# Kernel optimization log

Hardware: AMD Instinct MI355X
Metric: run time of the kernel (lower is better)

The kernel has to match this reference:

```python
import jax, jax.numpy as jnp
import numpy as np

MAX_NUM_LEVELS = 3.5
NUM_LEVELS = 4  # mip levels 0..3 (levels clamped to [0, 2.5])


def affine_grid(matrix, N, H, W):
    # F.affine_grid, align_corners=False. matrix: (N,2,3) -> grid (N,H,W,2) in xy order.
    xs = (jnp.arange(W, dtype=jnp.float32) + 0.5) * (2.0 / W) - 1.0
    ys = (jnp.arange(H, dtype=jnp.float32) + 0.5) * (2.0 / H) - 1.0
    gy, gx = jnp.meshgrid(ys, xs, indexing='ij')
    base = jnp.stack([gx, gy, jnp.ones_like(gx)], axis=-1)  # (H,W,3)
    return jnp.einsum('hwk,nik->nhwi', base, matrix)  # (N,H,W,2)


def grid_sample_border(img, grid):
    # bilinear grid_sample, padding_mode='border', align_corners=False
    N, C, H, W = img.shape
    x = (grid[..., 0] + 1.0) * (W / 2.0) - 0.5
    y = (grid[..., 1] + 1.0) * (H / 2.0) - 0.5
    x0 = jnp.floor(x); y0 = jnp.floor(y)
    tx = x - x0; ty = y - y0
    x0i = jnp.clip(x0.astype(jnp.int32), 0, W - 1)
    x1i = jnp.clip(x0.astype(jnp.int32) + 1, 0, W - 1)
    y0i = jnp.clip(y0.astype(jnp.int32), 0, H - 1)
    y1i = jnp.clip(y0.astype(jnp.int32) + 1, 0, H - 1)
    b = jnp.arange(N)[:, None, None]
    g = lambda yi, xi: img[b, :, yi, xi]  # (N,Ho,Wo,C) gather
    out = (g(y0i, x0i) * ((1 - tx) * (1 - ty))[..., None]
           + g(y0i, x1i) * (tx * (1 - ty))[..., None]
           + g(y1i, x0i) * ((1 - tx) * ty)[..., None]
           + g(y1i, x1i) * (tx * ty)[..., None])
    return jnp.transpose(out, (0, 3, 1, 2))  # (N,C,Ho,Wo)


def blur_downsample(x):
    N, C, H, W = x.shape
    k1 = jnp.array([1., 3., 3., 1.], dtype=x.dtype) / 8.0
    k = k1[:, None] * k1[None, :]
    xp = jnp.pad(x, ((0, 0), (0, 0), (1, 2), (1, 2)), mode='reflect')
    kernel = jnp.broadcast_to(k[None, None], (C, 1, 4, 4))
    return jax.lax.conv_general_dilated(xp, kernel, window_strides=(2, 2), padding='VALID',
                                        feature_group_count=C,
                                        dimension_numbers=('NCHW', 'OIHW', 'NCHW'))


def compute_levels(grid, H, W):
    # per-pixel mip LOD from local stretch of the sampling grid (in source pixel units)
    coords = (grid + 1.0) * 0.5 * jnp.array([W, H], dtype=grid.dtype)  # (N,Ho,Wo,2)
    dx = coords[:, :-1, 1:] - coords[:, :-1, :-1]
    dy = coords[:, 1:, :-1] - coords[:, :-1, :-1]
    scale = jnp.maximum(jnp.linalg.norm(dx, axis=-1), jnp.linalg.norm(dy, axis=-1))
    scale = jnp.pad(scale, ((0, 0), (0, 1), (0, 1)), mode='edge')  # (N,Ho,Wo)
    levels = jnp.log2(jnp.maximum(scale, 1.0))
    return jnp.clip(levels, 0.0, MAX_NUM_LEVELS - 1.0)


def mipmap_warp(img, grid):
    N, C, H, W = img.shape
    levels = compute_levels(grid, H, W)  # (N,Ho,Wo)
    pyr = [img]
    for _ in range(NUM_LEVELS - 1):
        pyr.append(blur_downsample(pyr[-1]))
    samples = jnp.stack([grid_sample_border(p, grid) for p in pyr], axis=0)  # (L,N,C,Ho,Wo)
    ls = jnp.arange(NUM_LEVELS, dtype=levels.dtype)[:, None, None, None]
    w = jnp.clip(1.0 - jnp.abs(levels[None] - ls), 0.0, 1.0)  # trilinear blend weights (L,N,Ho,Wo)
    return jnp.einsum('lnhw,lnchw->nchw', w, samples)


def setup_inputs() -> dict:
    key = jax.random.key(0)
    k1, k2, k3 = jax.random.split(key, 3)
    N, C, H, W, D = 64, 3, 256, 256, 512
    img = jax.random.normal(k1, (N, C, H, W), dtype=jnp.float32)
    features = jax.random.normal(k2, (N, D), dtype=jnp.float32)
    # learned head params (zero-init in torch; small random here so the warp is nontrivial)
    lin_w = jax.random.normal(k3, (4, D), dtype=jnp.float32) * 0.02
    lin_b = jnp.zeros((4,), dtype=jnp.float32)
    return {'img': img, 'features': features, 'lin_w': lin_w, 'lin_b': lin_b}


def reference(img, features, lin_w, lin_b):
    params = features @ lin_w.T + lin_b  # (N,4)
    rot = jnp.tanh(params[:, 0:1]) * jnp.pi
    scale = jnp.exp(params[:, 1:2])
    sx, sy = params[:, 2:3], params[:, 3:4]
    c, s = jnp.cos(rot), jnp.sin(rot)
    matrix = jnp.concatenate([scale * c, -scale * s, sx, scale * s, scale * c, sy], axis=1).reshape(-1, 2, 3)
    affine_params = jnp.concatenate([rot, scale, sx, sy], axis=1)
    N, C, H, W = img.shape
    grid = affine_grid(matrix, N, H, W)
    out = mipmap_warp(img, grid)
    return out, grid, matrix, affine_params
```

## Files before the change

### kernel.cpp

```cpp
#include <hip/hip_runtime.h>
#include <math.h>

#define N_B 64
#define C_CH 3
#define H_IMG 256
#define W_IMG 256
#define D_FEAT 512

#define OUT_OFF_GRID   12582912
#define OUT_OFF_MATRIX 20971520
#define OUT_OFF_AFFINE 20971904

#define PYR1_SZ (N_B * 128 * 128 * 3)
#define PYR2_SZ (N_B * 64 * 64 * 3)
#define PYR3_SZ (N_B * 32 * 32 * 3)

typedef float v2f __attribute__((ext_vector_type(2)));
typedef float v4f __attribute__((ext_vector_type(4)));
typedef float f4u __attribute__((ext_vector_type(4), aligned(4)));
typedef float f2u __attribute__((ext_vector_type(2), aligned(4)));

__global__ void params_kernel(const float* __restrict__ features,
                              const float* __restrict__ lin_w,
                              const float* __restrict__ lin_b,
                              float* __restrict__ out_matrix,
                              float* __restrict__ out_affine,
                              float* __restrict__ ws_params)
{
    const int n = blockIdx.x;
    const int t = threadIdx.x;
    const float* f = features + n * D_FEAT;
    float f0 = f[t];
    float f1 = f[t + 256];
    float a0 = f0 * lin_w[0 * D_FEAT + t] + f1 * lin_w[0 * D_FEAT + t + 256];
    float a1 = f0 * lin_w[1 * D_FEAT + t] + f1 * lin_w[1 * D_FEAT + t + 256];
    float a2 = f0 * lin_w[2 * D_FEAT + t] + f1 * lin_w[2 * D_FEAT + t + 256];
    float a3 = f0 * lin_w[3 * D_FEAT + t] + f1 * lin_w[3 * D_FEAT + t + 256];

    __shared__ float red[4][256];
    red[0][t] = a0; red[1][t] = a1; red[2][t] = a2; red[3][t] = a3;
    __syncthreads();
    for (int s = 128; s > 0; s >>= 1) {
        if (t < s) {
            red[0][t] += red[0][t + s];
            red[1][t] += red[1][t + s];
            red[2][t] += red[2][t + s];
            red[3][t] += red[3][t + s];
        }
        __syncthreads();
    }
    if (t == 0) {
        float p0 = red[0][0] + lin_b[0];
        float p1 = red[1][0] + lin_b[1];
        float p2 = red[2][0] + lin_b[2];
        float p3 = red[3][0] + lin_b[3];
        float rot   = tanhf(p0) * 3.14159265358979323846f;
        float scale = expf(p1);
        float c = cosf(rot), s = sinf(rot);
        float m00 = scale * c, m01 = -scale * s, m02 = p2;
        float m10 = scale * s, m11 =  scale * c, m12 = p3;
        out_matrix[n * 6 + 0] = m00;
        out_matrix[n * 6 + 1] = m01;
        out_matrix[n * 6 + 2] = m02;
        out_matrix[n * 6 + 3] = m10;
        out_matrix[n * 6 + 4] = m11;
        out_matrix[n * 6 + 5] = m12;
        out_affine[n * 4 + 0] = rot;
        out_affine[n * 4 + 1] = scale;
        out_affine[n * 4 + 2] = p2;
        out_affine[n * 4 + 3] = p3;
        float lv = log2f(fmaxf(scale, 1.0f));
        lv = fminf(fmaxf(lv, 0.0f), 2.5f);
        ws_params[n * 8 + 0] = m00;
        ws_params[n * 8 + 1] = m01;
        ws_params[n * 8 + 2] = m02;
        ws_params[n * 8 + 3] = m10;
        ws_params[n * 8 + 4] = m11;
        ws_params[n * 8 + 5] = m12;
        ws_params[n * 8 + 6] = lv;
        ws_params[n * 8 + 7] = 0.0f;
    }
}

__global__ void down1_kernel(const float* __restrict__ img,
                             float* __restrict__ pyr1,
                             const float* __restrict__ ws_params)
{
    const int n = blockIdx.y;
    if (ws_params[n * 8 + 6] <= 0.0f) return;
    const int p = blockIdx.x * 256 + threadIdx.x;
    const int i = p >> 7;
    const int j = p & 127;

    int r[4];
#pragma unroll
    for (int a = 0; a < 4; a++) {
        int q = 2 * i + a - 1;
        if (q < 0) q = -q;
        if (q >= 256) q = 510 - q;
        r[a] = q;
    }
    const int  cb  = min(max(2 * j - 1, 0), 252);
    const bool jlo = (j == 0);
    const bool jhi = (j == 127);
    const bool je  = jlo || jhi;

    const float* s = img + (size_t)n * 3 * 65536;

    f4u T[3][4];
#pragma unroll
    for (int c = 0; c < 3; c++)
#pragma unroll
        for (int a = 0; a < 4; a++)
            T[c][a] = *(const f4u*)(s + c * 65536 + r[a] * 256 + cb);

    const float k0 = 0.125f, k1 = 0.375f;
    const float kr[4] = {0.125f, 0.375f, 0.375f, 0.125f};
    float o[3];
#pragma unroll
    for (int c = 0; c < 3; c++) {
        float acc = 0.0f;
#pragma unroll
        for (int a = 0; a < 4; a++) {
            f4u A = T[c][a];
            float t0 = je  ? A.y : A.x;
            float t1 = jlo ? A.x : (jhi ? A.z : A.y);
            float t2 = jlo ? A.y : (jhi ? A.w : A.z);
            float t3 = je  ? A.z : A.w;
            float h = k0 * t0 + k1 * t1 + k1 * t2 + k0 * t3;
            acc += kr[a] * h;
        }
        o[c] = acc;
    }
    float* d = pyr1 + (size_t)n * (128 * 128 * 3) + (size_t)p * 3;
    d[0] = o[0]; d[1] = o[1]; d[2] = o[2];
}

template<int Hs, int Ws>
__global__ void downN_kernel(const float* __restrict__ src,
                             float* __restrict__ dst,
                             const float* __restrict__ ws_params,
                             float lvl_gate)
{
    const int n = blockIdx.y;
    if (ws_params[n * 8 + 6] <= lvl_gate) return;
    constexpr int Hd = Hs / 2, Wd = Ws / 2;
    const int p = blockIdx.x * 256 + threadIdx.x;
    const int i = p / Wd;
    const int j = p % Wd;

    int r[4], cc[4];
#pragma unroll
    for (int a = 0; a < 4; a++) {
        int q = 2 * i + a - 1;
        if (q < 0) q = -q;
        if (q >= Hs) q = 2 * Hs - 2 - q;
        r[a] = q;
        int u = 2 * j + a - 1;
        if (u < 0) u = -u;
        if (u >= Ws) u = 2 * Ws - 2 - u;
        cc[a] = u;
    }
    const float* s = src + (size_t)n * 3 * Hs * Ws;
    const int rs = 3 * Ws;

    f4u T[4][4];
#pragma unroll
    for (int a = 0; a < 4; a++)
#pragma unroll
        for (int b = 0; b < 4; b++)
            T[a][b] = *(const f4u*)(s + r[a] * rs + 3 * cc[b]);

    const float k0 = 0.125f, k1 = 0.375f;
    const float kr[4] = {0.125f, 0.375f, 0.375f, 0.125f};
    float o[3];
#pragma unroll
    for (int c = 0; c < 3; c++) {
        float acc = 0.0f;
#pragma unroll
        for (int a = 0; a < 4; a++) {
            float h = k0 * T[a][0][c] + k1 * T[a][1][c]
                    + k1 * T[a][2][c] + k0 * T[a][3][c];
            acc += kr[a] * h;
        }
        o[c] = acc;
    }
    float* d = dst + (size_t)n * 3 * Hd * Wd + (size_t)p * 3;
    d[0] = o[0]; d[1] = o[1]; d[2] = o[2];
}

struct TapSetup {
    const float* row0;
    const float* row1;
    float w00, w01, w10, w11;
    bool selHi0, selLo1;
    size_t planeStride;
};

__device__ __forceinline__ TapSetup make_taps(const float* __restrict__ base, int l,
                                              float X, float Y)
{
    const int Wl = W_IMG >> l;
    const int Hl = H_IMG >> l;
    float x = (X + 1.0f) * (0.5f * (float)Wl) - 0.5f;
    float y = (Y + 1.0f) * (0.5f * (float)Hl) - 0.5f;
    float x0f = floorf(x), y0f = floorf(y);
    float tx = x - x0f, ty = y - y0f;
    int x0 = (int)x0f, y0 = (int)y0f;
    int y0i = min(max(y0,     0), Hl - 1);
    int y1i = min(max(y0 + 1, 0), Hl - 1);
    int xp = min(max(x0, 0), Wl - 2);
    TapSetup ts;
    ts.row0 = base + (size_t)y0i * Wl + xp;
    ts.row1 = base + (size_t)y1i * Wl + xp;
    ts.selHi0 = (x0 >= Wl - 1);
    ts.selLo1 = (x0 < 0);
    ts.w00 = (1.0f - tx) * (1.0f - ty);
    ts.w01 = tx * (1.0f - ty);
    ts.w10 = (1.0f - tx) * ty;
    ts.w11 = tx * ty;
    ts.planeStride = (size_t)Hl * Wl;
    return ts;
}

__device__ __forceinline__ float tap_eval(const TapSetup& ts, float2 a, float2 b)
{
    float t00 = ts.selHi0 ? a.y : a.x;
    float t01 = ts.selLo1 ? a.x : a.y;
    float t10 = ts.selHi0 ? b.y : b.x;
    float t11 = ts.selLo1 ? b.x : b.y;
    return ts.w00 * t00 + ts.w01 * t01 + ts.w10 * t10 + ts.w11 * t11;
}

struct NTap {
    const float* r0;
    const float* r1;
    float w00, w01, w10, w11;
    bool hi, lo;
};

__device__ __forceinline__ NTap make_ntap(const float* __restrict__ base, int l,
                                          float X, float Y)
{
    const int Wl = W_IMG >> l;
    const int Hl = H_IMG >> l;
    float x = (X + 1.0f) * (0.5f * (float)Wl) - 0.5f;
    float y = (Y + 1.0f) * (0.5f * (float)Hl) - 0.5f;
    float x0f = floorf(x), y0f = floorf(y);
    float tx = x - x0f, ty = y - y0f;
    int x0 = (int)x0f, y0 = (int)y0f;
    int y0i = min(max(y0,     0), Hl - 1);
    int y1i = min(max(y0 + 1, 0), Hl - 1);
    int xp  = min(max(x0, 0), Wl - 2);
    const int rs = 3 * Wl;
    NTap t;
    t.r0 = base + (size_t)y0i * rs + 3 * xp;
    t.r1 = base + (size_t)y1i * rs + 3 * xp;
    t.hi = (x0 >= Wl - 1);
    t.lo = (x0 < 0);
    t.w00 = (1.0f - tx) * (1.0f - ty);
    t.w01 = tx * (1.0f - ty);
    t.w10 = (1.0f - tx) * ty;
    t.w11 = tx * ty;
    return t;
}

struct NPay { f4u a; f2u a2; f4u b; f2u b2; };

__device__ __forceinline__ NPay ntap_load(const NTap& t)
{
    NPay p;
    p.a  = *(const f4u*)t.r0;  p.a2 = *(const f2u*)(t.r0 + 4);
    p.b  = *(const f4u*)t.r1;  p.b2 = *(const f2u*)(t.r1 + 4);
    return p;
}

__device__ __forceinline__ void ntap_eval(const NTap& t, const NPay& p, float* v)
{
    float e0[6] = {p.a.x, p.a.y, p.a.z, p.a.w, p.a2.x, p.a2.y};
    float e1[6] = {p.b.x, p.b.y, p.b.z, p.b.w, p.b2.x, p.b2.y};
#pragma unroll
    for (int c = 0; c < 3; c++) {
        float p00 = t.hi ? e0[c + 3] : e0[c];
        float p01 = t.lo ? e0[c]     : e0[c + 3];
        float p10 = t.hi ? e1[c + 3] : e1[c];
        float p11 = t.lo ? e1[c]     : e1[c + 3];
        v[c] = t.w00 * p00 + t.w01 * p01 + t.w10 * p10 + t.w11 * p11;
    }
}

__device__ __forceinline__ const float* npyr(int l, const float* p1,
                                             const float* p2, const float* p3,
                                             int n)
{
    if (l == 1) return p1 + (size_t)n * (128 * 128 * 3);
    if (l == 2) return p2 + (size_t)n * (64 * 64 * 3);
    return p3 + (size_t)n * (32 * 32 * 3);
}

__global__ __launch_bounds__(256, 4)
void warp_kernel(const float* __restrict__ img,
                 const float* __restrict__ pyr1,
                 const float* __restrict__ pyr2,
                 const float* __restrict__ pyr3,
                 const float* __restrict__ ws_params,
                 float* __restrict__ out,
                 float* __restrict__ gridOut)
{
    const int n = blockIdx.y;
    const int tile = blockIdx.x;
    const int tid = threadIdx.x;
    const int w0 = (tile & 7) << 5;
    const int h0 = (tile >> 3) << 4;
    const int w  = w0 + ((tid & 15) << 1);
    const int h  = h0 + (tid >> 4);

    const float* P = ws_params + n * 8;
    float m00 = P[0], m01 = P[1], m02 = P[2];
    float m10 = P[3], m11 = P[4], m12 = P[5];
    float lv  = P[6];

    float gxa = ((float)w + 0.5f) * (2.0f / (float)W_IMG) - 1.0f;
    float gxb = ((float)(w + 1) + 0.5f) * (2.0f / (float)W_IMG) - 1.0f;
    float gy  = ((float)h + 0.5f) * (2.0f / (float)H_IMG) - 1.0f;
    float Xa = m00 * gxa + m01 * gy + m02;
    float Ya = m10 * gxa + m11 * gy + m12;
    float Xb = m00 * gxb + m01 * gy + m02;
    float Yb = m10 * gxb + m11 * gy + m12;

    v4f gp = {Xa, Ya, Xb, Yb};
    __builtin_nontemporal_store(gp,
        (v4f*)(gridOut + ((size_t)(n * H_IMG + h) * W_IMG + w) * 2));

    int   l0   = (int)lv;
    float frac = lv - (float)l0;
    const bool hasL1 = (frac > 0.0f);
    const float wA = 1.0f - frac;

    size_t obase = ((size_t)n * C_CH * H_IMG + h) * W_IMG + w;

    if (l0 == 0) {
        const float* base0 = img + (size_t)n * 3 * 65536;
        TapSetup ta = make_taps(base0, 0, Xa, Ya);
        TapSetup tb = make_taps(base0, 0, Xb, Yb);
        float2 Aa[3], Ba[3], Ab[3], Bb[3];
#pragma unroll
        for (int c = 0; c < 3; c++) {
            Aa[c] = *(const float2*)(ta.row0 + c * 65536);
            Ba[c] = *(const float2*)(ta.row1 + c * 65536);
            Ab[c] = *(const float2*)(tb.row0 + c * 65536);
            Bb[c] = *(const float2*)(tb.row1 + c * 65536);
        }
        if (hasL1) {
            const float* b1 = pyr1 + (size_t)n * (128 * 128 * 3);
            NTap ua = make_ntap(b1, 1, Xa, Ya);
            NTap ub = make_ntap(b1, 1, Xb, Yb);
            NPay pa = ntap_load(ua);
            NPay pb = ntap_load(ub);
            float v1a[3], v1b[3];
            ntap_eval(ua, pa, v1a);
            ntap_eval(ub, pb, v1b);
#pragma unroll
            for (int c = 0; c < 3; c++) {
                float v0a = tap_eval(ta, Aa[c], Ba[c]);
                float v0b = tap_eval(tb, Ab[c], Bb[c]);
                v2f o2 = {wA * v0a + frac * v1a[c], wA * v0b + frac * v1b[c]};
                __builtin_nontemporal_store(o2,
                    (v2f*)(out + obase + (size_t)c * 65536));
            }
        } else {
#pragma unroll
            for (int c = 0; c < 3; c++) {
                v2f o2 = {tap_eval(ta, Aa[c], Ba[c]), tap_eval(tb, Ab[c], Bb[c])};
                __builtin_nontemporal_store(o2,
                    (v2f*)(out + obase + (size_t)c * 65536));
            }
        }
    } else {
        const float* base0 = npyr(l0, pyr1, pyr2, pyr3, n);
        NTap ta = make_ntap(base0, l0, Xa, Ya);
        NTap tb = make_ntap(base0, l0, Xb, Yb);
        NPay pa = ntap_load(ta);
        NPay pb = ntap_load(tb);
        if (hasL1) {
            const float* base1 = npyr(l0 + 1, pyr1, pyr2, pyr3, n);
            NTap ua = make_ntap(base1, l0 + 1, Xa, Ya);
            NTap ub = make_ntap(base1, l0 + 1, Xb, Yb);
            NPay qa = ntap_load(ua);
            NPay qb = ntap_load(ub);
            float v0a[3], v0b[3], v1a[3], v1b[3];
            ntap_eval(ta, pa, v0a);
            ntap_eval(tb, pb, v0b);
            ntap_eval(ua, qa, v1a);
            ntap_eval(ub, qb, v1b);
#pragma unroll
            for (int c = 0; c < 3; c++) {
                v2f o2 = {wA * v0a[c] + frac * v1a[c], wA * v0b[c] + frac * v1b[c]};
                __builtin_nontemporal_store(o2,
                    (v2f*)(out + obase + (size_t)c * 65536));
            }
        } else {
            float v0a[3], v0b[3];
            ntap_eval(ta, pa, v0a);
            ntap_eval(tb, pb, v0b);
#pragma unroll
            for (int c = 0; c < 3; c++) {
                v2f o2 = {v0a[c], v0b[c]};
                __builtin_nontemporal_store(o2,
                    (v2f*)(out + obase + (size_t)c * 65536));
            }
        }
    }
}

extern "C" void kernel_launch(void* const* d_in, const int* in_sizes, int n_in,
                              void* d_out, int out_size, void* d_ws, size_t ws_size,
                              hipStream_t stream)
{
    const float* img      = (const float*)d_in[0];
    const float* features = (const float*)d_in[1];
    const float* lin_w    = (const float*)d_in[2];
    const float* lin_b    = (const float*)d_in[3];

    float* out        = (float*)d_out;
    float* gridOut    = out + OUT_OFF_GRID;
    float* out_matrix = out + OUT_OFF_MATRIX;
    float* out_affine = out + OUT_OFF_AFFINE;

    float* ws        = (float*)d_ws;
    float* ws_params = ws;
    float* pyr1 = ws + 1024;
    float* pyr2 = pyr1 + PYR1_SZ;
    float* pyr3 = pyr2 + PYR2_SZ;

    params_kernel<<<N_B, 256, 0, stream>>>(features, lin_w, lin_b,
                                           out_matrix, out_affine, ws_params);

    down1_kernel<<<dim3(64, N_B), 256, 0, stream>>>(img, pyr1, ws_params);
    downN_kernel<128, 128><<<dim3(16, N_B), 256, 0, stream>>>(pyr1, pyr2, ws_params, 1.0f);
    downN_kernel<64, 64><<<dim3(4, N_B), 256, 0, stream>>>(pyr2, pyr3, ws_params, 2.0f);

    warp_kernel<<<dim3(H_IMG * W_IMG / 512, N_B), 256, 0, stream>>>(
        img, pyr1, pyr2, pyr3, ws_params, out, gridOut);
}
```

Before: 164.5 us.

## Stage level-0 source footprint into LDS for warp tile bilinear sampling

For level-0 tiles, each block computes the bounding box of its 32x16 output tile's source footprint. If the box fits the 36 KB LDS buffer, the block cooperatively copies the three channel patches into LDS, synchronises, and does the bilinear taps from shared memory instead of scattered global float2 loads. The aim is to replace redundant, poorly coalesced gathers with coalesced row loads plus cheap LDS reads. In exchange it adds a __syncthreads, extra copy work when the footprint is large, and 36 KB of static LDS per block, which may cut occupancy below the launch_bounds target of 4 blocks.

```diff
diff --git a/kernel.cpp b/kernel.cpp
--- a/kernel.cpp
+++ b/kernel.cpp
@@ -14,6 +14,8 @@
 #define PYR1_SZ (N_B * 128 * 128 * 3)
 #define PYR2_SZ (N_B * 64 * 64 * 3)
 #define PYR3_SZ (N_B * 32 * 32 * 3)
+
+#define LDS_CAP 3072
 
 typedef float v2f __attribute__((ext_vector_type(2)));
 typedef float v4f __attribute__((ext_vector_type(4)));
@@ -232,6 +234,50 @@
     return ts.w00 * t00 + ts.w01 * t01 + ts.w10 * t10 + ts.w11 * t11;
 }
 
+struct STap {
+    int off0, off1;
+    float w00, w01, w10, w11;
+    bool hi, lo;
+};
+
+__device__ __forceinline__ STap make_stap(float X, float Y,
+                                          int bx0, int by0, int bwp)
+{
+    float x = (X + 1.0f) * 128.0f - 0.5f;
+    float y = (Y + 1.0f) * 128.0f - 0.5f;
+    float x0f = floorf(x), y0f = floorf(y);
+    float tx = x - x0f, ty = y - y0f;
+    int x0 = (int)x0f, y0 = (int)y0f;
+    int y0i = min(max(y0,     0), 255);
+    int y1i = min(max(y0 + 1, 0), 255);
+    int xp  = min(max(x0, 0), 254);
+    STap t;
+    t.off0 = (y0i - by0) * bwp + (xp - bx0);
+    t.off1 = (y1i - by0) * bwp + (xp - bx0);
+    t.hi = (x0 >= 255);
+    t.lo = (x0 < 0);
+    t.w00 = (1.0f - tx) * (1.0f - ty);
+    t.w01 = tx * (1.0f - ty);
+    t.w10 = (1.0f - tx) * ty;
+    t.w11 = tx * ty;
+    return t;
+}
+
+__device__ __forceinline__ void stap_eval(const float (*L)[LDS_CAP],
+                                          const STap& t, float* v)
+{
+#pragma unroll
+    for (int c = 0; c < 3; c++) {
+        f2u a = *(const f2u*)&L[c][t.off0];
+        f2u b = *(const f2u*)&L[c][t.off1];
+        float t00 = t.hi ? a.y : a.x;
+        float t01 = t.lo ? a.x : a.y;
+        float t10 = t.hi ? b.y : b.x;
+        float t11 = t.lo ? b.x : b.y;
+        v[c] = t.w00 * t00 + t.w01 * t01 + t.w10 * t10 + t.w11 * t11;
+    }
+}
+
 struct NTap {
     const float* r0;
     const float* r1;
@@ -307,6 +353,8 @@
                  float* __restrict__ out,
                  float* __restrict__ gridOut)
 {
+    __shared__ float lds[3][LDS_CAP];
+
     const int n = blockIdx.y;
     const int tile = blockIdx.x;
     const int tid = threadIdx.x;
@@ -340,38 +388,93 @@
     size_t obase = ((size_t)n * C_CH * H_IMG + h) * W_IMG + w;
 
     if (l0 == 0) {
-        const float* base0 = img + (size_t)n * 3 * 65536;
-        TapSetup ta = make_taps(base0, 0, Xa, Ya);
-        TapSetup tb = make_taps(base0, 0, Xb, Yb);
-        float2 Aa[3], Ba[3], Ab[3], Bb[3];
-#pragma unroll
-        for (int c = 0; c < 3; c++) {
-            Aa[c] = *(const float2*)(ta.row0 + c * 65536);
-            Ba[c] = *(const float2*)(ta.row1 + c * 65536);
-            Ab[c] = *(const float2*)(tb.row0 + c * 65536);
-            Bb[c] = *(const float2*)(tb.row1 + c * 65536);
-        }
+        float cgxl = ((float)w0 + 0.5f) * (2.0f / (float)W_IMG) - 1.0f;
+        float cgxr = ((float)(w0 + 31) + 0.5f) * (2.0f / (float)W_IMG) - 1.0f;
+        float cgyt = ((float)h0 + 0.5f) * (2.0f / (float)H_IMG) - 1.0f;
+        float cgyb = ((float)(h0 + 15) + 0.5f) * (2.0f / (float)H_IMG) - 1.0f;
+        float x00 = (m00 * cgxl + m01 * cgyt + m02 + 1.0f) * 128.0f - 0.5f;
+        float x01 = (m00 * cgxr + m01 * cgyt + m02 + 1.0f) * 128.0f - 0.5f;
+        float x10 = (m00 * cgxl + m01 * cgyb + m02 + 1.0f) * 128.0f - 0.5f;
+        float x11 = (m00 * cgxr + m01 * cgyb + m02 + 1.0f) * 128.0f - 0.5f;
+        float y00 = (m10 * cgxl + m11 * cgyt + m12 + 1.0f) * 128.0f - 0.5f;
+        float y01 = (m10 * cgxr + m11 * cgyt + m12 + 1.0f) * 128.0f - 0.5f;
+        float y10 = (m10 * cgxl + m11 * cgyb + m12 + 1.0f) * 128.0f - 0.5f;
+        float y11 = (m10 * cgxr + m11 * cgyb + m12 + 1.0f) * 128.0f - 0.5f;
+        float xmn = fminf(fminf(x00, x01), fminf(x10, x11));
+        float xmx = fmaxf(fmaxf(x00, x01), fmaxf(x10, x11));
+        float ymn = fminf(fminf(y00, y01), fminf(y10, y11));
+        float ymx = fmaxf(fmaxf(y00, y01), fmaxf(y10, y11));
+        int bx0 = min(max((int)floorf(xmn), 0), 255);
+        int bx1 = min(max((int)floorf(xmx) + 1, 0), 255);
+        int by0 = min(max((int)floorf(ymn), 0), 255);
+        int by1 = min(max((int)floorf(ymx) + 1, 0), 255);
+        int bw  = bx1 - bx0 + 1;
+        int bh  = by1 - by0 + 1;
+        int bwp = bw | 1;
+        const bool staged = (bh * bwp <= LDS_CAP);
+
+        NTap ua, ub; NPay pa, pb;
         if (hasL1) {
             const float* b1 = pyr1 + (size_t)n * (128 * 128 * 3);
-            NTap ua = make_ntap(b1, 1, Xa, Ya);
-            NTap ub = make_ntap(b1, 1, Xb, Yb);
-            NPay pa = ntap_load(ua);
-            NPay pb = ntap_load(ub);
+            ua = make_ntap(b1, 1, Xa, Ya);
+            ub = make_ntap(b1, 1, Xb, Yb);
+            pa = ntap_load(ua);
+            pb = ntap_load(ub);
+        }
+
+        float v0a[3], v0b[3];
+        if (staged) {
+            const int cr = tid & 31;
+            const int rr = tid >> 5;
+            const float* sbase = img + (size_t)n * 3 * 65536;
+#pragma unroll
+            for (int c = 0; c < 3; c++) {
+                const float* cp = sbase + c * 65536;
+                for (int r = rr; r < bh; r += 8) {
+                    const float* rowp = cp + (by0 + r) * 256 + bx0;
+                    float* lp = &lds[c][r * bwp];
+                    for (int col = cr; col < bw; col += 32)
+                        lp[col] = rowp[col];
+                }
+            }
+            __syncthreads();
+            STap sa = make_stap(Xa, Ya, bx0, by0, bwp);
+            STap sb = make_stap(Xb, Yb, bx0, by0, bwp);
+            stap_eval(lds, sa, v0a);
+            stap_eval(lds, sb, v0b);
+        } else {
+            const float* base0 = img + (size_t)n * 3 * 65536;
+            TapSetup ta = make_taps(base0, 0, Xa, Ya);
+            TapSetup tb = make_taps(base0, 0, Xb, Yb);
+            float2 Aa[3], Ba[3], Ab[3], Bb[3];
+#pragma unroll
+            for (int c = 0; c < 3; c++) {
+                Aa[c] = *(const float2*)(ta.row0 + c * 65536);
+                Ba[c] = *(const float2*)(ta.row1 + c * 65536);
+                Ab[c] = *(const float2*)(tb.row0 + c * 65536);
+                Bb[c] = *(const float2*)(tb.row1 + c * 65536);
+            }
+#pragma unroll
+            for (int c = 0; c < 3; c++) {
+                v0a[c] = tap_eval(ta, Aa[c], Ba[c]);
+                v0b[c] = tap_eval(tb, Ab[c], Bb[c]);
+            }
+        }
+
+        if (hasL1) {
             float v1a[3], v1b[3];
             ntap_eval(ua, pa, v1a);
             ntap_eval(ub, pb, v1b);
 #pragma unroll
             for (int c = 0; c < 3; c++) {
-                float v0a = tap_eval(ta, Aa[c], Ba[c]);
-                float v0b = tap_eval(tb, Ab[c], Bb[c]);
-                v2f o2 = {wA * v0a + frac * v1a[c], wA * v0b + frac * v1b[c]};
+                v2f o2 = {wA * v0a[c] + frac * v1a[c], wA * v0b[c] + frac * v1b[c]};
                 __builtin_nontemporal_store(o2,
                     (v2f*)(out + obase + (size_t)c * 65536));
             }
         } else {
 #pragma unroll
             for (int c = 0; c < 3; c++) {
-                v2f o2 = {tap_eval(ta, Aa[c], Ba[c]), tap_eval(tb, Ab[c], Bb[c])};
+                v2f o2 = {v0a[c], v0b[c]};
                 __builtin_nontemporal_store(o2,
                     (v2f*)(out + obase + (size_t)c * 65536));
             }
```

After: 186.8 us. 13.5% more time.

## Transpose level-0 image to NHWC so warp gathers channels contiguously

Applied to the files above, without the earlier changes.

Adds a pre-pass that rewrites the full-resolution image from planar NCHW into interleaved NHWC in the workspace, for batch items whose mip level is below 1. The warp kernel then samples level 0 through the same interleaved-tap path already used for pyramid levels, loading all three channels per tap in one access instead of three planar loads. It falls back to the old planar path when the workspace is too small. The trade-off is an extra full read and write of the image, which must be recovered by cheaper gathers in the warp kernel.

```diff
diff --git a/kernel.cpp b/kernel.cpp
--- a/kernel.cpp
+++ b/kernel.cpp
@@ -14,6 +14,7 @@
 #define PYR1_SZ (N_B * 128 * 128 * 3)
 #define PYR2_SZ (N_B * 64 * 64 * 3)
 #define PYR3_SZ (N_B * 32 * 32 * 3)
+#define IMGT_SZ (N_B * 256 * 256 * 3)
 
 typedef float v2f __attribute__((ext_vector_type(2)));
 typedef float v4f __attribute__((ext_vector_type(4)));
@@ -82,6 +83,28 @@
     }
 }
 
+__global__ void nhwc0_kernel(const float* __restrict__ img,
+                             float* __restrict__ imgT,
+                             const float* __restrict__ ws_params)
+{
+    const int n = blockIdx.y;
+    if (ws_params[n * 8 + 6] >= 1.0f) return;
+    const int idx = blockIdx.x * 256 + threadIdx.x;
+    const int i = idx >> 6;
+    const int t = idx & 63;
+    const float* s = img + (size_t)n * 3 * 65536 + i * 256 + 4 * t;
+    f4u v0 = *(const f4u*)(s);
+    f4u v1 = *(const f4u*)(s + 65536);
+    f4u v2 = *(const f4u*)(s + 131072);
+    float* d = imgT + (size_t)n * (256 * 256 * 3) + ((size_t)i * 256 + 4 * t) * 3;
+    f4u s0 = {v0.x, v1.x, v2.x, v0.y};
+    f4u s1 = {v1.y, v2.y, v0.z, v1.z};
+    f4u s2 = {v2.z, v0.w, v1.w, v2.w};
+    *(f4u*)(d)     = s0;
+    *(f4u*)(d + 4) = s1;
+    *(f4u*)(d + 8) = s2;
+}
+
 __global__ void down1_kernel(const float* __restrict__ img,
                              float* __restrict__ pyr1,
                              const float* __restrict__ ws_params)
@@ -289,17 +312,20 @@
     }
 }
 
-__device__ __forceinline__ const float* npyr(int l, const float* p1,
-                                             const float* p2, const float* p3,
-                                             int n)
-{
+__device__ __forceinline__ const float* npyr0(int l, const float* iT,
+                                              const float* p1, const float* p2,
+                                              const float* p3, int n)
+{
+    if (l == 0) return iT + (size_t)n * (256 * 256 * 3);
     if (l == 1) return p1 + (size_t)n * (128 * 128 * 3);
     if (l == 2) return p2 + (size_t)n * (64 * 64 * 3);
     return p3 + (size_t)n * (32 * 32 * 3);
 }
 
+template<bool NHWC0>
 __global__ __launch_bounds__(256, 4)
 void warp_kernel(const float* __restrict__ img,
+                 const float* __restrict__ imgT,
                  const float* __restrict__ pyr1,
                  const float* __restrict__ pyr2,
                  const float* __restrict__ pyr3,
@@ -339,7 +365,41 @@
 
     size_t obase = ((size_t)n * C_CH * H_IMG + h) * W_IMG + w;
 
-    if (l0 == 0) {
+    if (NHWC0 || l0 != 0) {
+        const float* base0 = npyr0(l0, imgT, pyr1, pyr2, pyr3, n);
+        NTap ta = make_ntap(base0, l0, Xa, Ya);
+        NTap tb = make_ntap(base0, l0, Xb, Yb);
+        NPay pa = ntap_load(ta);
+        NPay pb = ntap_load(tb);
+        if (hasL1) {
+            const float* base1 = npyr0(l0 + 1, imgT, pyr1, pyr2, pyr3, n);
+            NTap ua = make_ntap(base1, l0 + 1, Xa, Ya);
+            NTap ub = make_ntap(base1, l0 + 1, Xb, Yb);
+            NPay qa = ntap_load(ua);
+            NPay qb = ntap_load(ub);
+            float v0a[3], v0b[3], v1a[3], v1b[3];
+            ntap_eval(ta, pa, v0a);
+            ntap_eval(tb, pb, v0b);
+            ntap_eval(ua, qa, v1a);
+            ntap_eval(ub, qb, v1b);
+#pragma unroll
+            for (int c = 0; c < 3; c++) {
+                v2f o2 = {wA * v0a[c] + frac * v1a[c], wA * v0b[c] + frac * v1b[c]};
+                __builtin_nontemporal_store(o2,
+                    (v2f*)(out + obase + (size_t)c * 65536));
+            }
+        } else {
+            float v0a[3], v0b[3];
+            ntap_eval(ta, pa, v0a);
+            ntap_eval(tb, pb, v0b);
+#pragma unroll
+            for (int c = 0; c < 3; c++) {
+                v2f o2 = {v0a[c], v0b[c]};
+                __builtin_nontemporal_store(o2,
+                    (v2f*)(out + obase + (size_t)c * 65536));
+            }
+        }
+    } else {
         const float* base0 = img + (size_t)n * 3 * 65536;
         TapSetup ta = make_taps(base0, 0, Xa, Ya);
         TapSetup tb = make_taps(base0, 0, Xb, Yb);
@@ -376,40 +436,6 @@
                     (v2f*)(out + obase + (size_t)c * 65536));
             }
         }
-    } else {
-        const float* base0 = npyr(l0, pyr1, pyr2, pyr3, n);
-        NTap ta = make_ntap(base0, l0, Xa, Ya);
-        NTap tb = make_ntap(base0, l0, Xb, Yb);
-        NPay pa = ntap_load(ta);
-        NPay pb = ntap_load(tb);
-        if (hasL1) {
-            const float* base1 = npyr(l0 + 1, pyr1, pyr2, pyr3, n);
-            NTap ua = make_ntap(base1, l0 + 1, Xa, Ya);
-            NTap ub = make_ntap(base1, l0 + 1, Xb, Yb);
-            NPay qa = ntap_load(ua);
-            NPay qb = ntap_load(ub);
-            float v0a[3], v0b[3], v1a[3], v1b[3];
-            ntap_eval(ta, pa, v0a);
-            ntap_eval(tb, pb, v0b);
-            ntap_eval(ua, qa, v1a);
-            ntap_eval(ub, qb, v1b);
-#pragma unroll
-            for (int c = 0; c < 3; c++) {
-                v2f o2 = {wA * v0a[c] + frac * v1a[c], wA * v0b[c] + frac * v1b[c]};
-                __builtin_nontemporal_store(o2,
-                    (v2f*)(out + obase + (size_t)c * 65536));
-            }
-        } else {
-            float v0a[3], v0b[3];
-            ntap_eval(ta, pa, v0a);
-            ntap_eval(tb, pb, v0b);
-#pragma unroll
-            for (int c = 0; c < 3; c++) {
-                v2f o2 = {v0a[c], v0b[c]};
-                __builtin_nontemporal_store(o2,
-                    (v2f*)(out + obase + (size_t)c * 65536));
-            }
-        }
     }
 }
 
@@ -432,14 +458,25 @@
     float* pyr1 = ws + 1024;
     float* pyr2 = pyr1 + PYR1_SZ;
     float* pyr3 = pyr2 + PYR2_SZ;
+    float* imgT = pyr3 + PYR3_SZ;
+
+    const size_t need_floats = 1024 + (size_t)PYR1_SZ + PYR2_SZ + PYR3_SZ + IMGT_SZ;
+    const bool useT = ws_size >= need_floats * sizeof(float);
 
     params_kernel<<<N_B, 256, 0, stream>>>(features, lin_w, lin_b,
                                            out_matrix, out_affine, ws_params);
+
+    if (useT)
+        nhwc0_kernel<<<dim3(64, N_B), 256, 0, stream>>>(img, imgT, ws_params);
 
     down1_kernel<<<dim3(64, N_B), 256, 0, stream>>>(img, pyr1, ws_params);
     downN_kernel<128, 128><<<dim3(16, N_B), 256, 0, stream>>>(pyr1, pyr2, ws_params, 1.0f);
     downN_kernel<64, 64><<<dim3(4, N_B), 256, 0, stream>>>(pyr2, pyr3, ws_params, 2.0f);
 
-    warp_kernel<<<dim3(H_IMG * W_IMG / 512, N_B), 256, 0, stream>>>(
-        img, pyr1, pyr2, pyr3, ws_params, out, gridOut);
-}
+    if (useT)
+        warp_kernel<true><<<dim3(H_IMG * W_IMG / 512, N_B), 256, 0, stream>>>(
+            img, imgT, pyr1, pyr2, pyr3, ws_params, out, gridOut);
+    else
+        warp_kernel<false><<<dim3(H_IMG * W_IMG / 512, N_B), 256, 0, stream>>>(
+            img, imgT, pyr1, pyr2, pyr3, ws_params, out, gridOut);
+}
```

After: 170.1 us. +3.4%, slower.
